# Kernel optimization log

Measured on AMD Instinct MI355X. Metric: run time of the kernel, lower is better.

Reference implementation:

```python
import jax, jax.numpy as jnp
import numpy as np
import math

EPS = 1e-6
MAX_NORM = 1.0 - 1e-3


def _clip_to_ball(x):
    # Keep point strictly inside the unit ball (||x|| < 1).
    norm = jnp.maximum(jnp.linalg.norm(x, axis=-1, keepdims=True), EPS)
    factor = jnp.minimum(MAX_NORM / norm, 1.0)
    return x * factor


def setup_inputs() -> dict:
    key = jax.random.key(0)
    k1, k2 = jax.random.split(key)
    B, C, D = 8192, 4096, 512
    euclidean_emb = jax.random.normal(k1, (B, D), dtype=jnp.float32)
    centroids = jax.random.uniform(k2, (C, D), dtype=jnp.float32, minval=-0.01, maxval=0.01)
    log_c = jnp.asarray(math.log(1.0), dtype=jnp.float32)
    return {"euclidean_emb": euclidean_emb, "log_c": log_c, "centroids": centroids}


def reference(euclidean_emb, log_c, centroids):
    # torch code used c = self.log_c.exp().item() -> c is detached scalar
    c = jax.lax.stop_gradient(jnp.exp(log_c))
    sqrt_c = jnp.sqrt(c)

    # expmap0: Euclidean -> Poincare ball
    v_norm = jnp.maximum(jnp.linalg.norm(euclidean_emb, axis=-1, keepdims=True), EPS)
    coeff = jnp.tanh(sqrt_c * v_norm) / (sqrt_c * v_norm)
    x_h = _clip_to_ball(coeff * euclidean_emb)   # (B, D)
    cen_h = _clip_to_ball(centroids)             # (C, D)

    # Pairwise Poincare distance via GEMM (same math as the expanded (B,C,D) form):
    # ||x - y||^2 = ||x||^2 + ||y||^2 - 2 <x, y>
    x2_raw = jnp.sum(x_h * x_h, axis=-1)         # (B,)
    y2_raw = jnp.sum(cen_h * cen_h, axis=-1)     # (C,)
    x2 = jnp.minimum(x2_raw, MAX_NORM ** 2)
    y2 = jnp.minimum(y2_raw, MAX_NORM ** 2)
    xy = x_h @ cen_h.T                           # (B, C) GEMM
    diff2 = x2_raw[:, None] + y2_raw[None, :] - 2.0 * xy

    denom = jnp.maximum((1.0 - c * x2)[:, None] * (1.0 - c * y2)[None, :], EPS)
    arg = jnp.maximum(1.0 + c * (2.0 * diff2) / denom, 1.0 + EPS)
    dists = jnp.arccosh(arg) / sqrt_c            # (B, C)
    return dists, x_h, cen_h
```

## Files before the change

### kernel.cpp

```cpp
#include <hip/hip_runtime.h>
#include <math.h>

#define EPSV 1e-6f
#define MAX_NORM (1.0f - 1e-3f)

typedef __attribute__((ext_vector_type(8))) short short8;
typedef __attribute__((ext_vector_type(4))) float f32x4;

__device__ inline ushort f32_to_bf16(float f) {
    union { float f; uint32_t u; } cv;
    cv.f = f;
    uint32_t u = cv.u;
    u += 0x7FFFu + ((u >> 16) & 1u);
    return (ushort)(u >> 16);
}

__device__ inline void glds16(const ushort* gsrc, ushort* ldsdst) {
    auto* g = (const __attribute__((address_space(1))) uint32_t*)gsrc;
    auto* l = (__attribute__((address_space(3))) uint32_t*)ldsdst;
    __builtin_amdgcn_global_load_lds(g, l, 16, 0, 0);
}

__device__ inline short8 ds_read128(const ushort* p) {
    auto* l3 = (const __attribute__((address_space(3))) ushort*)p;
    const uint32_t addr = (uint32_t)(uintptr_t)l3;
    short8 v;
    asm volatile("ds_read_b128 %0, %1" : "=&v"(v) : "v"(addr));
    return v;
}

__device__ inline short8 gload16(const ushort* p) {
    short8 v;
    asm volatile("global_load_dwordx4 %0, %1, off" : "=&v"(v) : "v"(p));
    return v;
}

__device__ inline size_t pack_off(int r, int j) {
    return ((size_t)(r >> 4) * 16 + (j >> 2)) * 512
         + (size_t)(((j & 3) * 16 + (r & 15)) * 8);
}

__global__ void rows_emb_kernel(const float* __restrict__ emb,
                                const float* __restrict__ logc,
                                float* __restrict__ xh,
                                ushort* __restrict__ xpk,
                                float* __restrict__ x2raw,
                                float* __restrict__ dxv) {
    const int D = 512;
    const int row = blockIdx.x;
    const int lane = threadIdx.x;

    const float4* r4 = (const float4*)(emb + (size_t)row * D);
    float4 a = r4[2 * lane];
    float4 b = r4[2 * lane + 1];

    float ss = a.x * a.x + a.y * a.y + a.z * a.z + a.w * a.w
             + b.x * b.x + b.y * b.y + b.z * b.z + b.w * b.w;
#pragma unroll
    for (int off = 32; off > 0; off >>= 1) ss += __shfl_xor(ss, off, 64);

    const float c  = expf(logc[0]);
    const float sc = sqrtf(c);

    const float tn    = sqrtf(ss);
    const float vn    = fmaxf(tn, EPSV);
    const float coeff = tanhf(sc * vn) / (sc * vn);
    const float pre   = coeff * tn;
    const float fac   = fminf(MAX_NORM / fmaxf(pre, EPSV), 1.0f);
    const float scale = coeff * fac;

    float4 oa, ob;
    oa.x = a.x * scale; oa.y = a.y * scale; oa.z = a.z * scale; oa.w = a.w * scale;
    ob.x = b.x * scale; ob.y = b.y * scale; ob.z = b.z * scale; ob.w = b.w * scale;

    float4* o4 = (float4*)(xh + (size_t)row * D);
    o4[2 * lane]     = oa;
    o4[2 * lane + 1] = ob;

    union { ushort u[8]; uint4 v; } pk;
    pk.u[0] = f32_to_bf16(oa.x); pk.u[1] = f32_to_bf16(oa.y);
    pk.u[2] = f32_to_bf16(oa.z); pk.u[3] = f32_to_bf16(oa.w);
    pk.u[4] = f32_to_bf16(ob.x); pk.u[5] = f32_to_bf16(ob.y);
    pk.u[6] = f32_to_bf16(ob.z); pk.u[7] = f32_to_bf16(ob.w);
    *(uint4*)(xpk + pack_off(row, lane)) = pk.v;

    if (lane == 0) {
        const float sq = scale * scale * ss;
        x2raw[row] = sq;
        dxv[row]   = 1.0f - c * fminf(sq, MAX_NORM * MAX_NORM);
    }
}

__global__ void rows_cen_kernel(const float* __restrict__ cen,
                                const float* __restrict__ logc,
                                float* __restrict__ ch,
                                ushort* __restrict__ cpk,
                                float* __restrict__ y2raw,
                                float* __restrict__ dyv) {
    const int D = 512;
    const int row = blockIdx.x;
    const int lane = threadIdx.x;

    const float4* r4 = (const float4*)(cen + (size_t)row * D);
    float4 a = r4[2 * lane];
    float4 b = r4[2 * lane + 1];

    float ss = a.x * a.x + a.y * a.y + a.z * a.z + a.w * a.w
             + b.x * b.x + b.y * b.y + b.z * b.z + b.w * b.w;
#pragma unroll
    for (int off = 32; off > 0; off >>= 1) ss += __shfl_xor(ss, off, 64);

    const float c = expf(logc[0]);

    const float tn    = sqrtf(ss);
    const float scale = fminf(MAX_NORM / fmaxf(tn, EPSV), 1.0f);

    float4 oa, ob;
    oa.x = a.x * scale; oa.y = a.y * scale; oa.z = a.z * scale; oa.w = a.w * scale;
    ob.x = b.x * scale; ob.y = b.y * scale; ob.z = b.z * scale; ob.w = b.w * scale;

    float4* o4 = (float4*)(ch + (size_t)row * D);
    o4[2 * lane]     = oa;
    o4[2 * lane + 1] = ob;

    union { ushort u[8]; uint4 v; } pk;
    pk.u[0] = f32_to_bf16(oa.x); pk.u[1] = f32_to_bf16(oa.y);
    pk.u[2] = f32_to_bf16(oa.z); pk.u[3] = f32_to_bf16(oa.w);
    pk.u[4] = f32_to_bf16(ob.x); pk.u[5] = f32_to_bf16(ob.y);
    pk.u[6] = f32_to_bf16(ob.z); pk.u[7] = f32_to_bf16(ob.w);
    *(uint4*)(cpk + pack_off(row, lane)) = pk.v;

    if (lane == 0) {
        const float sq = scale * scale * ss;
        y2raw[row] = sq;
        dyv[row]   = 1.0f - c * fminf(sq, MAX_NORM * MAX_NORM);
    }
}

#define EPST 68
#define KDIM 512
#define NT 16
#define NCOLS 4096

__global__ __launch_bounds__(256, 3)
void gemm_epi_kernel(const ushort* __restrict__ Apk,
                     const ushort* __restrict__ Bpk,
                     const float* __restrict__ x2raw,
                     const float* __restrict__ dxv,
                     const float* __restrict__ y2raw,
                     const float* __restrict__ dyv,
                     const float* __restrict__ logc,
                     float* __restrict__ out) {
    __shared__ __align__(16) char smem[18432];
    ushort* Asm = (ushort*)smem;

    const int tid  = threadIdx.x;
    const int lane = tid & 63;
    const int wid  = tid >> 6;
    const int im   = wid >> 1;
    const int in   = wid & 1;

    const int bn = blockIdx.x;
    const int bm = blockIdx.y;

    f32x4 acc[4][4];
#pragma unroll
    for (int m = 0; m < 4; m++)
#pragma unroll
        for (int n = 0; n < 4; n++) acc[m][n] = (f32x4){0.f, 0.f, 0.f, 0.f};

    const ushort* gA0 = Apk + ((size_t)(bm * 8 + 2 * wid)) * 8192 + lane * 8;
    const ushort* gA1 = gA0 + 8192;
    ushort* lA = Asm + wid * 1024;

    const ushort* gB = Bpk + ((size_t)(bn * 8 + in * 4)) * 8192 + lane * 8;

    const ushort* rdA = Asm + im * 2048 + lane * 8;

    short8 bX[4], bY[4];

    glds16(gA0, lA);
    glds16(gA1, lA + 512);
#pragma unroll
    for (int n = 0; n < 4; n++) bX[n] = gload16(gB + n * 8192);

#define TILE_BODY(T, PAR, BCUR, BNXT)                                         \
    do {                                                                      \
        asm volatile("s_waitcnt vmcnt(0)" ::: "memory");                      \
        __builtin_amdgcn_sched_barrier(0);                                    \
        __builtin_amdgcn_s_barrier();                                         \
        if ((T) + 1 < NT) {                                                   \
            const int ko = ((T) + 1) * 512;                                   \
            BNXT[0] = gload16(gB + 0 * 8192 + ko);                            \
            BNXT[1] = gload16(gB + 1 * 8192 + ko);                            \
            BNXT[2] = gload16(gB + 2 * 8192 + ko);                            \
            BNXT[3] = gload16(gB + 3 * 8192 + ko);                            \
            glds16(gA0 + ko, lA + (((T) + 1) & 1) * 4096);                    \
            glds16(gA1 + ko, lA + (((T) + 1) & 1) * 4096 + 512);              \
        }                                                                     \
        const ushort* rA = rdA + (PAR) * 4096;                                \
        short8 a0 = ds_read128(rA);                                           \
        short8 a1 = ds_read128(rA + 512);                                     \
        short8 a2 = ds_read128(rA + 1024);                                    \
        short8 a3 = ds_read128(rA + 1536);                                    \
        asm volatile("s_waitcnt lgkmcnt(2)" ::: "memory");                    \
        __builtin_amdgcn_sched_barrier(0);                                    \
        __builtin_amdgcn_s_setprio(1);                                        \
        _Pragma("unroll")                                                     \
        for (int n = 0; n < 4; n++) {                                         \
            acc[0][n] = __builtin_amdgcn_mfma_f32_16x16x32_bf16(              \
                a0, BCUR[n], acc[0][n], 0, 0, 0);                             \
            acc[1][n] = __builtin_amdgcn_mfma_f32_16x16x32_bf16(              \
                a1, BCUR[n], acc[1][n], 0, 0, 0);                             \
        }                                                                     \
        __builtin_amdgcn_sched_barrier(0);                                    \
        __builtin_amdgcn_s_setprio(0);                                        \
        asm volatile("s_waitcnt lgkmcnt(0)" ::: "memory");                    \
        __builtin_amdgcn_sched_barrier(0);                                    \
        __builtin_amdgcn_s_setprio(1);                                        \
        _Pragma("unroll")                                                     \
        for (int n = 0; n < 4; n++) {                                         \
            acc[2][n] = __builtin_amdgcn_mfma_f32_16x16x32_bf16(              \
                a2, BCUR[n], acc[2][n], 0, 0, 0);                             \
            acc[3][n] = __builtin_amdgcn_mfma_f32_16x16x32_bf16(              \
                a3, BCUR[n], acc[3][n], 0, 0, 0);                             \
        }                                                                     \
        __builtin_amdgcn_sched_barrier(0);                                    \
        __builtin_amdgcn_s_setprio(0);                                        \
    } while (0)

#pragma unroll 1
    for (int i = 0; i < NT / 2; ++i) {
        const int te = 2 * i;
        TILE_BODY(te,     0, bX, bY);
        TILE_BODY(te + 1, 1, bY, bX);
    }
#undef TILE_BODY

    __syncthreads();

    const float c   = expf(logc[0]);
    const float rsc = 1.0f / sqrtf(c);
    const int l16 = lane & 15;
    const int lg  = lane >> 4;

    float* ep = (float*)(smem + (size_t)wid * 4352);
    const int gr_base = bm * 128 + im * 64;
    const int gc_base = bn * 128 + in * 64;

#pragma unroll
    for (int m = 0; m < 4; m++) {
#pragma unroll
        for (int n = 0; n < 4; n++)
#pragma unroll
            for (int r = 0; r < 4; r++)
                ep[(lg * 4 + r) * EPST + n * 16 + l16] = acc[m][n][r];
        asm volatile("s_waitcnt lgkmcnt(0)" ::: "memory");

#pragma unroll
        for (int it = 0; it < 4; it++) {
            const int row = it * 4 + lg;
            const int gr  = gr_base + m * 16 + row;
            const int gc  = gc_base + l16 * 4;
            float4 xy4 = *(const float4*)&ep[row * EPST + l16 * 4];
            const float rx  = x2raw[gr];
            const float dxr = dxv[gr];
            const float4 ry4 = *(const float4*)&y2raw[gc];
            const float4 dy4 = *(const float4*)&dyv[gc];
            float4 o;
            {
                const float rden = __builtin_amdgcn_rcpf(fmaxf(dxr * dy4.x, EPSV));
                float t = fmaxf(2.0f * c * (rx + ry4.x - 2.0f * xy4.x) * rden, EPSV);
                o.x = __logf(1.0f + t + __builtin_amdgcn_sqrtf(t * (t + 2.0f))) * rsc;
            }
            {
                const float rden = __builtin_amdgcn_rcpf(fmaxf(dxr * dy4.y, EPSV));
                float t = fmaxf(2.0f * c * (rx + ry4.y - 2.0f * xy4.y) * rden, EPSV);
                o.y = __logf(1.0f + t + __builtin_amdgcn_sqrtf(t * (t + 2.0f))) * rsc;
            }
            {
                const float rden = __builtin_amdgcn_rcpf(fmaxf(dxr * dy4.z, EPSV));
                float t = fmaxf(2.0f * c * (rx + ry4.z - 2.0f * xy4.z) * rden, EPSV);
                o.z = __logf(1.0f + t + __builtin_amdgcn_sqrtf(t * (t + 2.0f))) * rsc;
            }
            {
                const float rden = __builtin_amdgcn_rcpf(fmaxf(dxr * dy4.w, EPSV));
                float t = fmaxf(2.0f * c * (rx + ry4.w - 2.0f * xy4.w) * rden, EPSV);
                o.w = __logf(1.0f + t + __builtin_amdgcn_sqrtf(t * (t + 2.0f))) * rsc;
            }
            *(float4*)&out[(size_t)gr * NCOLS + gc] = o;
        }
        asm volatile("s_waitcnt lgkmcnt(0)" ::: "memory");
    }
}

extern "C" void kernel_launch(void* const* d_in, const int* in_sizes, int n_in,
                              void* d_out, int out_size, void* d_ws, size_t ws_size,
                              hipStream_t stream) {
    const float* emb  = (const float*)d_in[0];
    const float* logc = (const float*)d_in[1];
    const float* cen  = (const float*)d_in[2];

    const int D = 512;
    const int B = in_sizes[0] / D;
    const int C = in_sizes[2] / D;

    float* out   = (float*)d_out;
    float* dists = out;
    float* xh    = out + (size_t)B * C;
    float* ch    = xh + (size_t)B * D;

    char* ws = (char*)d_ws;
    size_t off = 0;
    auto alloc = [&](size_t bytes) -> char* {
        char* p = ws + off;
        off += (bytes + 255) & ~(size_t)255;
        return p;
    };
    ushort* xpk   = (ushort*)alloc((size_t)B * D * sizeof(ushort));
    ushort* cpk   = (ushort*)alloc((size_t)C * D * sizeof(ushort));
    float*  x2raw = (float*)alloc((size_t)B * sizeof(float));
    float*  dxv   = (float*)alloc((size_t)B * sizeof(float));
    float*  y2raw = (float*)alloc((size_t)C * sizeof(float));
    float*  dyv   = (float*)alloc((size_t)C * sizeof(float));

    rows_emb_kernel<<<B, 64, 0, stream>>>(emb, logc, xh, xpk, x2raw, dxv);
    rows_cen_kernel<<<C, 64, 0, stream>>>(cen, logc, ch, cpk, y2raw, dyv);

    dim3 grid(C / 128, B / 128);
    gemm_epi_kernel<<<grid, 256, 0, stream>>>(xpk, cpk, x2raw, dxv, y2raw, dyv,
                                              logc, dists);
}
```

Before: 82.54 us.

## Deepen A-tile LDS pipeline to four buffers with prefetch distance two

```diff
diff --git a/kernel.cpp b/kernel.cpp
--- a/kernel.cpp
+++ b/kernel.cpp
@@ -151,7 +151,7 @@
                      const float* __restrict__ dyv,
                      const float* __restrict__ logc,
                      float* __restrict__ out) {
-    __shared__ __align__(16) char smem[18432];
+    __shared__ __align__(16) char smem[32768];
     ushort* Asm = (ushort*)smem;
 
     const int tid  = threadIdx.x;
@@ -179,26 +179,33 @@
 
     short8 bX[4], bY[4];
 
+#pragma unroll
+    for (int n = 0; n < 4; n++) bX[n] = gload16(gB + n * 8192);
     glds16(gA0, lA);
     glds16(gA1, lA + 512);
-#pragma unroll
-    for (int n = 0; n < 4; n++) bX[n] = gload16(gB + n * 8192);
-
-#define TILE_BODY(T, PAR, BCUR, BNXT)                                         \
+    glds16(gA0 + 512, lA + 4096);
+    glds16(gA1 + 512, lA + 4096 + 512);
+
+#define BODY(J, BUSE, BNXT)                                                   \
     do {                                                                      \
-        asm volatile("s_waitcnt vmcnt(0)" ::: "memory");                      \
+        const int t = tb + (J);                                               \
+        if (t < NT - 1) asm volatile("s_waitcnt vmcnt(2)" ::: "memory");      \
+        else            asm volatile("s_waitcnt vmcnt(0)" ::: "memory");      \
         __builtin_amdgcn_sched_barrier(0);                                    \
         __builtin_amdgcn_s_barrier();                                         \
-        if ((T) + 1 < NT) {                                                   \
-            const int ko = ((T) + 1) * 512;                                   \
-            BNXT[0] = gload16(gB + 0 * 8192 + ko);                            \
-            BNXT[1] = gload16(gB + 1 * 8192 + ko);                            \
-            BNXT[2] = gload16(gB + 2 * 8192 + ko);                            \
-            BNXT[3] = gload16(gB + 3 * 8192 + ko);                            \
-            glds16(gA0 + ko, lA + (((T) + 1) & 1) * 4096);                    \
-            glds16(gA1 + ko, lA + (((T) + 1) & 1) * 4096 + 512);              \
+        if (t + 1 < NT) {                                                     \
+            const int ko1 = (t + 1) * 512;                                    \
+            BNXT[0] = gload16(gB + 0 * 8192 + ko1);                           \
+            BNXT[1] = gload16(gB + 1 * 8192 + ko1);                           \
+            BNXT[2] = gload16(gB + 2 * 8192 + ko1);                           \
+            BNXT[3] = gload16(gB + 3 * 8192 + ko1);                           \
         }                                                                     \
-        const ushort* rA = rdA + (PAR) * 4096;                                \
+        if (t + 2 < NT) {                                                     \
+            const int ko2 = (t + 2) * 512;                                    \
+            glds16(gA0 + ko2, lA + (((J) + 2) & 3) * 4096);                   \
+            glds16(gA1 + ko2, lA + (((J) + 2) & 3) * 4096 + 512);             \
+        }                                                                     \
+        const ushort* rA = rdA + (J) * 4096;                                  \
         short8 a0 = ds_read128(rA);                                           \
         short8 a1 = ds_read128(rA + 512);                                     \
         short8 a2 = ds_read128(rA + 1024);                                    \
@@ -209,9 +216,9 @@
         _Pragma("unroll")                                                     \
         for (int n = 0; n < 4; n++) {                                         \
             acc[0][n] = __builtin_amdgcn_mfma_f32_16x16x32_bf16(              \
-                a0, BCUR[n], acc[0][n], 0, 0, 0);                             \
+                a0, BUSE[n], acc[0][n], 0, 0, 0);                             \
             acc[1][n] = __builtin_amdgcn_mfma_f32_16x16x32_bf16(              \
-                a1, BCUR[n], acc[1][n], 0, 0, 0);                             \
+                a1, BUSE[n], acc[1][n], 0, 0, 0);                             \
         }                                                                     \
         __builtin_amdgcn_sched_barrier(0);                                    \
         __builtin_amdgcn_s_setprio(0);                                        \
@@ -221,21 +228,23 @@
         _Pragma("unroll")                                                     \
         for (int n = 0; n < 4; n++) {                                         \
             acc[2][n] = __builtin_amdgcn_mfma_f32_16x16x32_bf16(              \
-                a2, BCUR[n], acc[2][n], 0, 0, 0);                             \
+                a2, BUSE[n], acc[2][n], 0, 0, 0);                             \
             acc[3][n] = __builtin_amdgcn_mfma_f32_16x16x32_bf16(              \
-                a3, BCUR[n], acc[3][n], 0, 0, 0);                             \
+                a3, BUSE[n], acc[3][n], 0, 0, 0);                             \
         }                                                                     \
         __builtin_amdgcn_sched_barrier(0);                                    \
         __builtin_amdgcn_s_setprio(0);                                        \
     } while (0)
 
 #pragma unroll 1
-    for (int i = 0; i < NT / 2; ++i) {
-        const int te = 2 * i;
-        TILE_BODY(te,     0, bX, bY);
-        TILE_BODY(te + 1, 1, bY, bX);
+    for (int i = 0; i < 4; ++i) {
+        const int tb = 4 * i;
+        BODY(0, bX, bY);
+        BODY(1, bY, bX);
+        BODY(2, bX, bY);
+        BODY(3, bY, bX);
     }
-#undef TILE_BODY
+#undef BODY
 
     __syncthreads();
 
```

New measurement: 83.80 us (median of 2 runs). About the same (+1.5%).
